# Kernel optimization log

Hardware: AMD Instinct MI355X
Metric: run time of the kernel (lower is better)

The kernel has to match this reference:

```python
import math
import jax, jax.numpy as jnp
import numpy as np

B, L, D, H = 4, 1024, 512, 8
DK = D // H

def setup_inputs() -> dict:
    key = jax.random.key(0)
    ks = jax.random.split(key, 12)
    s = 0.02
    return {
        "query": jax.random.normal(ks[0], (B, L, D), jnp.float32),
        "key": jax.random.normal(ks[1], (B, L, D), jnp.float32),
        "value": jax.random.normal(ks[2], (B, L, D), jnp.float32),
        "wq_w": jax.random.normal(ks[3], (D, D), jnp.float32) * s,
        "wq_b": jnp.zeros((D,), jnp.float32),
        "wk_w": jax.random.normal(ks[4], (D, D), jnp.float32) * s,
        "wk_b": jnp.zeros((D,), jnp.float32),
        "wv_w": jax.random.normal(ks[5], (D, D), jnp.float32) * s,
        "wv_b": jnp.zeros((D,), jnp.float32),
        "dense_w": jax.random.normal(ks[6], (D, D), jnp.float32) * s,
        "dense_b": jnp.zeros((D,), jnp.float32),
        "gate_w": jax.random.normal(ks[7], (D, 1), jnp.float32) * s,
        "gate_b": jnp.zeros((1,), jnp.float32),
        "mp_wq_w": jax.random.normal(ks[8], (D, D), jnp.float32) * s,
        "mp_wq_b": jnp.zeros((D,), jnp.float32),
        "mp_wk_w": jax.random.normal(ks[9], (D, D), jnp.float32) * s,
        "mp_wk_b": jnp.zeros((D,), jnp.float32),
    }

def reference(query, key, value, wq_w, wq_b, wk_w, wk_b, wv_w, wv_b,
              dense_w, dense_b, gate_w, gate_b,
              mp_wq_w, mp_wq_b, mp_wk_w, mp_wk_b):
    # Multi-head projections -> (B, H, L, DK)
    q = (query @ wq_w + wq_b).reshape(B, L, H, DK).transpose(0, 2, 1, 3)
    k = (key @ wk_w + wk_b).reshape(B, L, H, DK).transpose(0, 2, 1, 3)
    v = (value @ wv_w + wv_b).reshape(B, L, H, DK).transpose(0, 2, 1, 3)

    # MaskPerturbation on original (unprojected-into-heads) Q, K; scale by sqrt(d_model)
    qp = query @ mp_wq_w + mp_wq_b              # (B, L, D)
    kp = key @ mp_wk_w + mp_wk_b                # (B, L, D)
    m = jax.nn.sigmoid(jnp.einsum('bqd,bkd->bqk', qp, kp) / math.sqrt(D))  # (B, L, L)

    # Scaled dot-product attention (no mask)
    scores = jnp.einsum('bhqd,bhkd->bhqk', q, k) / math.sqrt(DK)  # (B, H, L, L)
    p_attn = jax.nn.softmax(scores, axis=-1)

    # Calibration: attn_cal = attn * exp(1 - m), combined with per-query gate, re-softmax
    attn_cal = p_attn * jnp.exp(1.0 - m[:, None])                 # (B, H, L, L)
    g = jax.nn.sigmoid(query @ gate_w + gate_b)[:, None]          # (B, 1, L, 1)
    attn_comb = g * p_attn + (1.0 - g) * attn_cal
    attn_final = jax.nn.softmax(attn_comb, axis=-1)

    out = jnp.einsum('bhqk,bhkd->bhqd', attn_final, v)            # (B, H, L, DK)
    out = out.transpose(0, 2, 1, 3).reshape(B, L, D)
    out = out @ dense_w + dense_b                                 # dropout p=0 (eval)
    return (out, m)
```

## Files before the change

### kernel.cpp

```cpp
#include <hip/hip_runtime.h>

#define B_  4
#define L_  1024
#define D_  512
#define H_  8
#define DK_ 64
#define BL_ (B_*L_)

typedef unsigned short us16;
typedef __attribute__((ext_vector_type(8))) short bf16x8;
typedef __attribute__((ext_vector_type(4))) float f32x4;

__device__ __forceinline__ float us2f(us16 u) {
  union { unsigned int i; float f; } x;
  x.i = ((unsigned int)u) << 16;
  return x.f;
}
__device__ __forceinline__ us16 f2us(float f) {
  union { float f; unsigned int i; } x;
  x.f = f;
  unsigned int r = x.i + 0x7FFFu + ((x.i >> 16) & 1u);
  return (us16)(r >> 16);
}
__device__ __forceinline__ us16 cvt_us(float f) { return f2us(f); }
__device__ __forceinline__ us16 cvt_us(us16 u) { return u; }
__device__ __forceinline__ float fexp2(float x) {
  return __builtin_amdgcn_exp2f(x);
}

#define MFMA(a, b, c) __builtin_amdgcn_mfma_f32_16x16x32_bf16(a, b, c, 0, 0, 0)

struct WT6 {
  const float* src[6];
  us16* dst[6];
};
__global__ __launch_bounds__(256) void prep(WT6 p, const float* __restrict__ query,
    const float* __restrict__ gw, const float* __restrict__ gb,
    float* __restrict__ g, us16* __restrict__ qb) {
  __shared__ us16 T[64][72];
  int id = blockIdx.x;
  const int t = threadIdx.x;
  if (id < 1024) {
    int row = id * 4 + (t >> 6);
    int lane = t & 63;
    float pz = 0.f;
    for (int d = lane; d < D_; d += 64) pz += query[(size_t)row * D_ + d] * gw[d];
#pragma unroll
    for (int off = 32; off; off >>= 1) pz += __shfl_down(pz, off);
    if (lane == 0) g[row] = 1.f / (1.f + __expf(-(pz + gb[0])));
    return;
  }
  if (id >= 1408) {
    size_t base = (size_t)(id - 1408) * 4096 + t * 16;
    const float* src = query + base;
    union { bf16x8 v; us16 u[8]; } a0, a1;
#pragma unroll
    for (int j = 0; j < 8; ++j) { a0.u[j] = f2us(src[j]); a1.u[j] = f2us(src[8 + j]); }
    *(bf16x8*)&qb[base] = a0.v;
    *(bf16x8*)&qb[base + 8] = a1.v;
    return;
  }
  id -= 1024;
  const int z = id >> 6;
  const int k0 = ((id >> 3) & 7) * 64, n0 = (id & 7) * 64;
  const float* __restrict__ W = p.src[z];
  us16* __restrict__ Wt = p.dst[z];
  {
    int r = t >> 2, c = (t & 3) * 16;
    const float* src = W + (size_t)(k0 + r) * 512 + n0 + c;
    union { bf16x8 v; us16 u[8]; } p0, p1;
#pragma unroll
    for (int j = 0; j < 8; ++j) { p0.u[j] = f2us(src[j]); p1.u[j] = f2us(src[8 + j]); }
    *(bf16x8*)&T[r][c] = p0.v;
    *(bf16x8*)&T[r][c + 8] = p1.v;
  }
  __syncthreads();
  {
    int n = t >> 2, c = (t & 3) * 16;
    union { bf16x8 v; us16 u[8]; } p0, p1;
#pragma unroll
    for (int j = 0; j < 8; ++j) { p0.u[j] = T[c + j][n]; p1.u[j] = T[c + 8 + j][n]; }
    us16* dst = Wt + (size_t)(n0 + n) * 512 + k0 + c;
    *(bf16x8*)dst = p0.v;
    *(bf16x8*)(dst + 8) = p1.v;
  }
}

__global__ __launch_bounds__(256) void gate_kernel(
    const float* __restrict__ query, const float* __restrict__ gw,
    const float* __restrict__ gb, float* __restrict__ g) {
  int row = blockIdx.x * 4 + (threadIdx.x >> 6);
  int lane = threadIdx.x & 63;
  float p = 0.f;
  for (int d = lane; d < D_; d += 64) p += query[(size_t)row * D_ + d] * gw[d];
#pragma unroll
  for (int off = 32; off; off >>= 1) p += __shfl_down(p, off);
  if (lane == 0) g[row] = 1.f / (1.f + __expf(-(p + gb[0])));
}

struct GJob {
  const float* A; const us16* Ab; const us16* Wt;
  const float* bias; us16* C; int mode; int atype;
};
struct GJobs { GJob j[3]; };

__global__ __launch_bounds__(256) void gemm3(GJobs jobs) {
  __shared__ us16 Al[64][72];
  __shared__ us16 Wl[64][72];
  int f = blockIdx.x + 8 * (blockIdx.y + 64 * blockIdx.z);
  const int cpx = 64 * (int)gridDim.z;
  f = (f & 7) * cpx + (f >> 3);
  const int bx = f & 7, by = (f >> 3) & 63, bz = f >> 9;
  const GJob J = jobs.j[bz];
  const int tid = threadIdx.x;
  const int w = tid >> 6, lane = tid & 63;
  const int quad = lane >> 4, lc = lane & 15;
  const int row0 = by * 64, col0 = bx * 64;
  const int sr = tid >> 2, sc = (tid & 3) * 16;
  f32x4 acc[4] = {};
  for (int k0 = 0; k0 < 512; k0 += 64) {
    if (J.atype) {
      const us16* as = J.Ab + (size_t)(row0 + sr) * 512 + k0 + sc;
      *(bf16x8*)&Al[sr][sc] = *(const bf16x8*)as;
      *(bf16x8*)&Al[sr][sc + 8] = *(const bf16x8*)(as + 8);
    } else {
      const float* as = J.A + (size_t)(row0 + sr) * 512 + k0 + sc;
      union { bf16x8 v; us16 u[8]; } p0, p1;
#pragma unroll
      for (int j = 0; j < 8; ++j) { p0.u[j] = f2us(as[j]); p1.u[j] = f2us(as[8 + j]); }
      *(bf16x8*)&Al[sr][sc] = p0.v;
      *(bf16x8*)&Al[sr][sc + 8] = p1.v;
    }
    {
      const us16* wsrc = J.Wt + (size_t)(col0 + sr) * 512 + k0 + sc;
      *(bf16x8*)&Wl[sr][sc] = *(const bf16x8*)wsrc;
      *(bf16x8*)&Wl[sr][sc + 8] = *(const bf16x8*)(wsrc + 8);
    }
    __syncthreads();
    bf16x8 a0 = *(const bf16x8*)&Al[w * 16 + lc][quad * 8];
    bf16x8 a1 = *(const bf16x8*)&Al[w * 16 + lc][32 + quad * 8];
#pragma unroll
    for (int ct = 0; ct < 4; ++ct) {
      bf16x8 b0 = *(const bf16x8*)&Wl[ct * 16 + lc][quad * 8];
      bf16x8 b1 = *(const bf16x8*)&Wl[ct * 16 + lc][32 + quad * 8];
      acc[ct] = MFMA(a0, b0, acc[ct]);
      acc[ct] = MFMA(a1, b1, acc[ct]);
    }
    __syncthreads();
  }
  const int orow = row0 + w * 16 + quad * 4;
#pragma unroll
  for (int ct = 0; ct < 4; ++ct) {
    const int col = col0 + ct * 16 + lc;
    const float bv = J.bias[col];
    if (J.mode == 0) {
#pragma unroll
      for (int r = 0; r < 4; ++r)
        J.C[(size_t)(orow + r) * 512 + col] = f2us(acc[ct][r] + bv);
    } else {
      const int h = col >> 6, dk = col & 63;
#pragma unroll
      for (int r = 0; r < 4; ++r) {
        const int grow = orow + r;
        const int b = grow >> 10, kv = grow & 1023;
        J.C[(((size_t)b * H_ + h) * DK_ + dk) * L_ + kv] = f2us(acc[ct][r] + bv);
      }
    }
  }
}

__global__ __launch_bounds__(256) void gemm_dense(
    const us16* __restrict__ A, const us16* __restrict__ Wt,
    const float* __restrict__ bias, float* __restrict__ C) {
  __shared__ us16 Al[64][72];
  __shared__ us16 Wl[64][72];
  int f = blockIdx.x + 8 * blockIdx.y;
  f = (f & 7) * 64 + (f >> 3);
  const int bx = f & 7, by = f >> 3;
  const int tid = threadIdx.x;
  const int w = tid >> 6, lane = tid & 63;
  const int quad = lane >> 4, lc = lane & 15;
  const int row0 = by * 64, col0 = bx * 64;
  const int sr = tid >> 2, sc = (tid & 3) * 16;
  f32x4 acc[4] = {};
  for (int k0 = 0; k0 < 512; k0 += 64) {
    const us16* as = A + (size_t)(row0 + sr) * 512 + k0 + sc;
    const us16* wsrc = Wt + (size_t)(col0 + sr) * 512 + k0 + sc;
    *(bf16x8*)&Al[sr][sc] = *(const bf16x8*)as;
    *(bf16x8*)&Al[sr][sc + 8] = *(const bf16x8*)(as + 8);
    *(bf16x8*)&Wl[sr][sc] = *(const bf16x8*)wsrc;
    *(bf16x8*)&Wl[sr][sc + 8] = *(const bf16x8*)(wsrc + 8);
    __syncthreads();
    bf16x8 a0 = *(const bf16x8*)&Al[w * 16 + lc][quad * 8];
    bf16x8 a1 = *(const bf16x8*)&Al[w * 16 + lc][32 + quad * 8];
#pragma unroll
    for (int ct = 0; ct < 4; ++ct) {
      bf16x8 b0 = *(const bf16x8*)&Wl[ct * 16 + lc][quad * 8];
      bf16x8 b1 = *(const bf16x8*)&Wl[ct * 16 + lc][32 + quad * 8];
      acc[ct] = MFMA(a0, b0, acc[ct]);
      acc[ct] = MFMA(a1, b1, acc[ct]);
    }
    __syncthreads();
  }
  const int orow = row0 + w * 16 + quad * 4;
#pragma unroll
  for (int ct = 0; ct < 4; ++ct) {
    const int col = col0 + ct * 16 + lc;
    const float bv = bias[col];
#pragma unroll
    for (int r = 0; r < 4; ++r)
      C[(size_t)(orow + r) * 512 + col] = acc[ct][r] + bv;
  }
}

template <bool WK>
__global__ __launch_bounds__(256) void mask16(
    const us16* __restrict__ QP, const us16* __restrict__ KP,
    float* __restrict__ Mout, const float* __restrict__ gbuf,
    us16* __restrict__ Wk) {
  __shared__ us16 Al[64][72];
  __shared__ us16 Bl[64][72];
  int f = blockIdx.x + 16 * (blockIdx.y + 16 * blockIdx.z);
  f = (f & 7) * 128 + (f >> 3);
  const int bx = f & 15, by = (f >> 4) & 15, b = f >> 8;
  const int tid = threadIdx.x;
  const int w = tid >> 6, lane = tid & 63;
  const int quad = lane >> 4, lc = lane & 15;
  const int row0 = by * 64, col0 = bx * 64;
  const us16* Ab = QP + (size_t)b * L_ * D_;
  const us16* Bb = KP + (size_t)b * L_ * D_;
  const int sr = tid >> 2, sc = (tid & 3) * 16;
  f32x4 acc[4] = {};
  for (int k0 = 0; k0 < 512; k0 += 64) {
    {
      const us16* as = Ab + (size_t)(row0 + sr) * 512 + k0 + sc;
      *(bf16x8*)&Al[sr][sc] = *(const bf16x8*)as;
      *(bf16x8*)&Al[sr][sc + 8] = *(const bf16x8*)(as + 8);
    }
    {
      const us16* bs = Bb + (size_t)(col0 + sr) * 512 + k0 + sc;
      *(bf16x8*)&Bl[sr][sc] = *(const bf16x8*)bs;
      *(bf16x8*)&Bl[sr][sc + 8] = *(const bf16x8*)(bs + 8);
    }
    __syncthreads();
    bf16x8 a0 = *(const bf16x8*)&Al[w * 16 + lc][quad * 8];
    bf16x8 a1 = *(const bf16x8*)&Al[w * 16 + lc][32 + quad * 8];
#pragma unroll
    for (int ct = 0; ct < 4; ++ct) {
      bf16x8 b0 = *(const bf16x8*)&Bl[ct * 16 + lc][quad * 8];
      bf16x8 b1 = *(const bf16x8*)&Bl[ct * 16 + lc][32 + quad * 8];
      acc[ct] = MFMA(a0, b0, acc[ct]);
      acc[ct] = MFMA(a1, b1, acc[ct]);
    }
    __syncthreads();
  }
  const float sc2 = 0.04419417382415922f;
  const int orow = row0 + w * 16 + quad * 4;
  float gq[4];
  if (WK) {
#pragma unroll
    for (int r = 0; r < 4; ++r) gq[r] = gbuf[b * L_ + orow + r];
  }
#pragma unroll
  for (int ct = 0; ct < 4; ++ct) {
    const int col = col0 + ct * 16 + lc;
#pragma unroll
    for (int r = 0; r < 4; ++r) {
      float x = acc[ct][r] * sc2;
      float v = 1.f / (1.f + __expf(-x));
      size_t idx = ((size_t)b * L_ + orow + r) * L_ + col;
      Mout[idx] = v;
      if (WK) Wk[idx] = f2us(gq[r] + (1.f - gq[r]) * __expf(1.f - v));
    }
  }
}

typedef const __attribute__((address_space(1))) unsigned int* gas_u32;
typedef __attribute__((address_space(3))) unsigned int* las_u32;

__global__ __launch_bounds__(256, 4) void attn8(
    const us16* Qp, const us16* __restrict__ Kp,
    const us16* __restrict__ Vt, const us16* __restrict__ Wk, us16* O) {
  __shared__ us16 P[16 * 1032];
  __shared__ float red[2][4][16];
  const int tid = threadIdx.x;
  const int w = tid >> 6, lane = tid & 63;
  const int quad = lane >> 4, lc = lane & 15;
  int raw = blockIdx.x + 64 * (blockIdx.y + 8 * blockIdx.z);
  const int c = raw & 7;
  const int rest = raw >> 3;
  const int gg = c * 4 + (rest & 3);
  const int q0 = (rest >> 2) * 16;
  const int h = gg & 7, b = gg >> 3;

  const us16* qptr = Qp + (size_t)(b * L_ + q0 + lc) * D_ + h * DK_;
  bf16x8 qa0 = *(const bf16x8*)(qptr + quad * 8);
  bf16x8 qa1 = *(const bf16x8*)(qptr + 32 + quad * 8);

  const us16* Kbase = Kp + (size_t)b * L_ * D_ + h * DK_;
  const int srow = lane >> 3;
  const int sblk = ((lane & 7) ^ srow) * 8;
  us16* kst = &P[w * 4096];

  auto stage = [&](int kt, int d) {
#pragma unroll
    for (int i = 0; i < 2; ++i) {
      const us16* src =
          Kbase + (size_t)(kt * 64 + w * 16 + i * 8 + srow) * D_ + sblk;
      __builtin_amdgcn_global_load_lds(
          (gas_u32)src, (las_u32)(kst + d * 1024 + i * 512), 16, 0, 0);
    }
  };

  const float c1 = 0.18033688011112042f;

  stage(0, 0); stage(1, 1); stage(2, 2); stage(3, 3);

  float s[16][4];
  float sm[4] = {0.f, 0.f, 0.f, 0.f};
#pragma unroll
  for (int kt = 0; kt < 16; ++kt) {
    const int d = kt & 3;
    if (kt <= 12)      asm volatile("s_waitcnt vmcnt(6)" ::: "memory");
    else if (kt == 13) asm volatile("s_waitcnt vmcnt(4)" ::: "memory");
    else if (kt == 14) asm volatile("s_waitcnt vmcnt(2)" ::: "memory");
    else               asm volatile("s_waitcnt vmcnt(0)" ::: "memory");
    __builtin_amdgcn_sched_barrier(0);
    bf16x8 b0 = *(const bf16x8*)&kst[d * 1024 + lc * 64 + ((quad ^ (lc & 7)) * 8)];
    bf16x8 b1 = *(const bf16x8*)&kst[d * 1024 + lc * 64 + (((4 + quad) ^ (lc & 7)) * 8)];
    if (kt + 4 < 16) stage(kt + 4, d);
    f32x4 a = {};
    __builtin_amdgcn_s_setprio(1);
    a = MFMA(qa0, b0, a);
    a = MFMA(qa1, b1, a);
    __builtin_amdgcn_s_setprio(0);
#pragma unroll
    for (int r = 0; r < 4; ++r) {
      float e = fexp2(a[r] * c1);
      s[kt][r] = e;
      sm[r] += e;
    }
    __builtin_amdgcn_sched_barrier(0);
  }
#pragma unroll
  for (int r = 0; r < 4; ++r)
#pragma unroll
    for (int off = 1; off < 16; off <<= 1) sm[r] += __shfl_xor(sm[r], off);
  if (lc == 0)
#pragma unroll
    for (int r = 0; r < 4; ++r) red[0][w][quad * 4 + r] = sm[r];
  __syncthreads();
  float invr[4];
#pragma unroll
  for (int r = 0; r < 4; ++r) {
    const int row = quad * 4 + r;
    invr[r] = 1.44269504088896341f /
              (red[0][0][row] + red[0][1][row] + red[0][2][row] + red[0][3][row]);
  }

  const us16* wkb = Wk + (size_t)(b * L_ + q0 + quad * 4) * L_ + w * 16 + lc;
  float ts[4] = {0.f, 0.f, 0.f, 0.f};
#pragma unroll
  for (int kt = 0; kt < 16; ++kt) {
#pragma unroll
    for (int r = 0; r < 4; ++r) {
      float cv = s[kt][r] * invr[r] * us2f(wkb[(size_t)r * L_ + kt * 64]);
      float e2 = fexp2(cv);
      ts[r] += e2;
      P[(quad * 4 + r) * 1032 + kt * 64 + w * 16 + lc] = f2us(e2);
    }
  }
#pragma unroll
  for (int r = 0; r < 4; ++r)
#pragma unroll
    for (int off = 1; off < 16; off <<= 1) ts[r] += __shfl_xor(ts[r], off);
  if (lc == 0)
#pragma unroll
    for (int r = 0; r < 4; ++r) red[1][w][quad * 4 + r] = ts[r];
  __syncthreads();

  const us16* Vb = Vt + ((size_t)(b * H_ + h) * DK_ + w * 16 + lc) * L_;
  f32x4 oacc = {};
  for (int kv = 0; kv < L_; kv += 32) {
    bf16x8 pa = *(const bf16x8*)&P[lc * 1032 + kv + quad * 8];
    bf16x8 vb = *(const bf16x8*)(Vb + kv + quad * 8);
    __builtin_amdgcn_s_setprio(1);
    oacc = MFMA(pa, vb, oacc);
    __builtin_amdgcn_s_setprio(0);
  }
#pragma unroll
  for (int r = 0; r < 4; ++r) {
    const int row = quad * 4 + r;
    float inv2 = 1.f /
        (red[1][0][row] + red[1][1][row] + red[1][2][row] + red[1][3][row]);
    O[(size_t)(b * L_ + q0 + row) * D_ + h * DK_ + w * 16 + lc] =
        f2us(oacc[r] * inv2);
  }
}

template <int MODE, typename TA>
__global__ __launch_bounds__(256) void gemm16(
    const TA* __restrict__ A, const float* __restrict__ W,
    const float* __restrict__ bias, void* __restrict__ Cout) {
  __shared__ us16 Al[64][56];
  __shared__ us16 Wl[64][56];
  const int tid = threadIdx.x;
  const int w = tid >> 6, lane = tid & 63;
  const int quad = lane >> 4, lc = lane & 15;
  const int row0 = blockIdx.y * 64, col0 = blockIdx.x * 64;
  f32x4 acc[4] = {};
  const int arow = tid >> 2, aks = (tid & 3) * 8;
  const int wk = tid & 31, wns = (tid >> 5) * 8;
  for (int k0 = 0; k0 < 512; k0 += 32) {
    {
      union { bf16x8 v; us16 u[8]; } pk;
      const TA* src = A + (size_t)(row0 + arow) * 512 + k0 + aks;
#pragma unroll
      for (int j = 0; j < 8; ++j) pk.u[j] = cvt_us(src[j]);
      *(bf16x8*)&Al[arow][aks] = pk.v;
    }
    {
      const float* src = W + (size_t)(k0 + wk) * 512 + col0 + wns;
#pragma unroll
      for (int j = 0; j < 8; ++j) Wl[wns + j][wk] = f2us(src[j]);
    }
    __syncthreads();
    bf16x8 af = *(const bf16x8*)&Al[w * 16 + lc][quad * 8];
#pragma unroll
    for (int ct = 0; ct < 4; ++ct) {
      bf16x8 bf = *(const bf16x8*)&Wl[ct * 16 + lc][quad * 8];
      acc[ct] = MFMA(af, bf, acc[ct]);
    }
    __syncthreads();
  }
  const int orow = row0 + w * 16 + quad * 4;
#pragma unroll
  for (int ct = 0; ct < 4; ++ct) {
    const int col = col0 + ct * 16 + lc;
    const float bv = bias[col];
    if (MODE == 0) {
      us16* C = (us16*)Cout;
#pragma unroll
      for (int r = 0; r < 4; ++r)
        C[(size_t)(orow + r) * 512 + col] = f2us(acc[ct][r] + bv);
    } else if (MODE == 1) {
      us16* C = (us16*)Cout;
      const int h = col >> 6, dk = col & 63;
#pragma unroll
      for (int r = 0; r < 4; ++r) {
        const int grow = orow + r;
        const int b = grow >> 10, kv = grow & 1023;
        C[(((size_t)b * H_ + h) * DK_ + dk) * L_ + kv] = f2us(acc[ct][r] + bv);
      }
    } else {
      float* C = (float*)Cout;
#pragma unroll
      for (int r = 0; r < 4; ++r)
        C[(size_t)(orow + r) * 512 + col] = acc[ct][r] + bv;
    }
  }
}

__global__ __launch_bounds__(256, 3) void attn2_fb(
    const us16* Qp, const us16* __restrict__ Kp,
    const us16* __restrict__ Vt, const float* __restrict__ Mm,
    const float* __restrict__ gbuf, us16* O) {
  __shared__ us16 Ql[16][72];
  __shared__ us16 P[16 * 1032];
  __shared__ float red[2][4][16];
  const int tid = threadIdx.x;
  const int w = tid >> 6, lane = tid & 63;
  const int quad = lane >> 4, lc = lane & 15;
  const int b = blockIdx.z, h = blockIdx.y, q0 = blockIdx.x * 16;
  if (tid < 128) {
    int r = tid >> 3, ks = (tid & 7) * 8;
    *(bf16x8*)&Ql[r][ks] =
        *(const bf16x8*)(Qp + (size_t)(b * L_ + q0 + r) * D_ + h * DK_ + ks);
  }
  __syncthreads();
  bf16x8 qa0 = *(const bf16x8*)&Ql[lc][quad * 8];
  bf16x8 qa1 = *(const bf16x8*)&Ql[lc][32 + quad * 8];
  const us16* Kbase = Kp + (size_t)b * L_ * D_ + h * DK_;
  float s[16][4];
#pragma unroll
  for (int kt = 0; kt < 16; ++kt) {
    const us16* kr = Kbase + (size_t)(kt * 64 + w * 16 + lc) * D_;
    bf16x8 b0 = *(const bf16x8*)(kr + quad * 8);
    bf16x8 b1 = *(const bf16x8*)(kr + 32 + quad * 8);
    f32x4 a = {};
    a = MFMA(qa0, b0, a);
    a = MFMA(qa1, b1, a);
#pragma unroll
    for (int r = 0; r < 4; ++r) s[kt][r] = a[r] * 0.125f;
  }
  float sm[4];
#pragma unroll
  for (int r = 0; r < 4; ++r) {
    float t = 0.f;
#pragma unroll
    for (int kt = 0; kt < 16; ++kt) { s[kt][r] = __expf(s[kt][r]); t += s[kt][r]; }
#pragma unroll
    for (int off = 1; off < 16; off <<= 1) t += __shfl_xor(t, off);
    sm[r] = t;
  }
  if (lc == 0)
#pragma unroll
    for (int r = 0; r < 4; ++r) red[0][w][quad * 4 + r] = sm[r];
  __syncthreads();
  float inv[4];
#pragma unroll
  for (int r = 0; r < 4; ++r) {
    const int row = quad * 4 + r;
    inv[r] = 1.f / (red[0][0][row] + red[0][1][row] + red[0][2][row] + red[0][3][row]);
  }
  float gq[4];
#pragma unroll
  for (int r = 0; r < 4; ++r) gq[r] = gbuf[b * L_ + q0 + quad * 4 + r];
#pragma unroll
  for (int r = 0; r < 4; ++r) {
    const float* mrow = Mm + (size_t)(b * L_ + q0 + quad * 4 + r) * L_;
    float t = 0.f;
#pragma unroll
    for (int kt = 0; kt < 16; ++kt) {
      float mval = mrow[kt * 64 + w * 16 + lc];
      float c = s[kt][r] * inv[r] * (gq[r] + (1.f - gq[r]) * __expf(1.f - mval));
      float e = __expf(c);
      s[kt][r] = e;
      t += e;
    }
#pragma unroll
    for (int off = 1; off < 16; off <<= 1) t += __shfl_xor(t, off);
    sm[r] = t;
  }
  if (lc == 0)
#pragma unroll
    for (int r = 0; r < 4; ++r) red[1][w][quad * 4 + r] = sm[r];
  __syncthreads();
#pragma unroll
  for (int r = 0; r < 4; ++r) {
    const int row = quad * 4 + r;
    inv[r] = 1.f / (red[1][0][row] + red[1][1][row] + red[1][2][row] + red[1][3][row]);
  }
#pragma unroll
  for (int kt = 0; kt < 16; ++kt)
#pragma unroll
    for (int r = 0; r < 4; ++r)
      P[(quad * 4 + r) * 1032 + kt * 64 + w * 16 + lc] = f2us(s[kt][r] * inv[r]);
  __syncthreads();
  const us16* Vb = Vt + (size_t)(b * H_ + h) * DK_ * L_;
  f32x4 oacc = {};
  for (int kv = 0; kv < L_; kv += 32) {
    bf16x8 pa = *(const bf16x8*)&P[lc * 1032 + kv + quad * 8];
    bf16x8 vb = *(const bf16x8*)(Vb + (size_t)(w * 16 + lc) * L_ + kv + quad * 8);
    oacc = MFMA(pa, vb, oacc);
  }
#pragma unroll
  for (int r = 0; r < 4; ++r)
    O[(size_t)(b * L_ + q0 + quad * 4 + r) * D_ + h * DK_ + w * 16 + lc] =
        f2us(oacc[r]);
}

extern "C" void kernel_launch(void* const* d_in, const int* in_sizes, int n_in,
                              void* d_out, int out_size, void* d_ws, size_t ws_size,
                              hipStream_t stream) {
  const float* query   = (const float*)d_in[0];
  const float* key     = (const float*)d_in[1];
  const float* value   = (const float*)d_in[2];
  const float* wq_w    = (const float*)d_in[3];
  const float* wq_b    = (const float*)d_in[4];
  const float* wk_w    = (const float*)d_in[5];
  const float* wk_b    = (const float*)d_in[6];
  const float* wv_w    = (const float*)d_in[7];
  const float* wv_b    = (const float*)d_in[8];
  const float* dense_w = (const float*)d_in[9];
  const float* dense_b = (const float*)d_in[10];
  const float* gate_w  = (const float*)d_in[11];
  const float* gate_b  = (const float*)d_in[12];
  const float* mp_wq_w = (const float*)d_in[13];
  const float* mp_wq_b = (const float*)d_in[14];
  const float* mp_wk_w = (const float*)d_in[15];
  const float* mp_wk_b = (const float*)d_in[16];

  const size_t RSZ = (size_t)BL_ * D_;
  const size_t WSZ = (size_t)D_ * D_;
  us16* R0 = (us16*)d_ws;
  us16* R1 = R0 + RSZ;

  float* out0 = (float*)d_out;
  float* outm = out0 + (size_t)B_ * L_ * D_;
  us16*  Vt   = (us16*)d_out;

  dim3 blk(256);

  if (ws_size >= ((size_t)20 << 20)) {
    us16* Wt0 = R1 + RSZ;
    us16* mpq_t = Wt0;
    us16* mpk_t = Wt0 + WSZ;
    us16* wq_t  = Wt0 + 2 * WSZ;
    us16* wk_t  = Wt0 + 3 * WSZ;
    us16* wv_t  = Wt0 + 4 * WSZ;
    us16* dw_t  = Wt0 + 5 * WSZ;
    us16* Wk    = Wt0 + 6 * WSZ;
    float* gbuf = (float*)(Wk + (size_t)B_ * L_ * L_);
    us16* qb = (us16*)((char*)d_out + (4u << 20));

    WT6 wt;
    wt.src[0] = mp_wq_w; wt.dst[0] = mpq_t;
    wt.src[1] = mp_wk_w; wt.dst[1] = mpk_t;
    wt.src[2] = wq_w;    wt.dst[2] = wq_t;
    wt.src[3] = wk_w;    wt.dst[3] = wk_t;
    wt.src[4] = wv_w;    wt.dst[4] = wv_t;
    wt.src[5] = dense_w; wt.dst[5] = dw_t;
    hipLaunchKernelGGL(prep, dim3(1920), blk, 0, stream, wt, query, gate_w, gate_b, gbuf, qb);

    GJobs mp;
    mp.j[0] = { nullptr, qb, mpq_t, mp_wq_b, R0, 0, 1 };
    mp.j[1] = { key, nullptr, mpk_t, mp_wk_b, R1, 0, 0 };
    mp.j[2] = mp.j[1];
    hipLaunchKernelGGL(gemm3, dim3(8, 64, 2), blk, 0, stream, mp);
    hipLaunchKernelGGL(mask16<true>, dim3(16, 16, B_), blk, 0, stream,
                       R0, R1, outm, gbuf, Wk);

    GJobs qkv;
    qkv.j[0] = { nullptr, qb, wq_t, wq_b, R0, 0, 1 };
    qkv.j[1] = { key, nullptr, wk_t, wk_b, R1, 0, 0 };
    qkv.j[2] = { value, nullptr, wv_t, wv_b, Vt, 1, 0 };
    hipLaunchKernelGGL(gemm3, dim3(8, 64, 3), blk, 0, stream, qkv);

    hipLaunchKernelGGL(attn8, dim3(L_ / 16, H_, B_), blk, 0, stream, R0, R1, Vt, Wk, R0);
    hipLaunchKernelGGL(gemm_dense, dim3(8, 64), blk, 0, stream, R0, dw_t, dense_b, out0);
  } else {
    float* gbuf = (float*)((char*)d_out + (4u << 20));
    dim3 gproj(8, 64);
    hipLaunchKernelGGL((gemm16<0, float>), gproj, blk, 0, stream, query, mp_wq_w, mp_wq_b, (void*)R0);
    hipLaunchKernelGGL((gemm16<0, float>), gproj, blk, 0, stream, key,   mp_wk_w, mp_wk_b, (void*)R1);
    hipLaunchKernelGGL(mask16<false>, dim3(16, 16, B_), blk, 0, stream,
                       R0, R1, outm, (const float*)nullptr, (us16*)nullptr);
    hipLaunchKernelGGL((gemm16<0, float>), gproj, blk, 0, stream, query, wq_w, wq_b, (void*)R0);
    hipLaunchKernelGGL((gemm16<0, float>), gproj, blk, 0, stream, key,   wk_w, wk_b, (void*)R1);
    hipLaunchKernelGGL((gemm16<1, float>), gproj, blk, 0, stream, value, wv_w, wv_b, (void*)Vt);
    hipLaunchKernelGGL(gate_kernel, dim3(BL_ / 4), blk, 0, stream, query, gate_w, gate_b, gbuf);
    hipLaunchKernelGGL(attn2_fb, dim3(L_ / 16, H_, B_), blk, 0, stream, R0, R1, Vt, outm, gbuf, R0);
    hipLaunchKernelGGL((gemm16<2, us16>), gproj, blk, 0, stream, R0, dense_w, dense_b, (void*)out0);
  }
}
```

Baseline: 222.1 us.

## Double-buffer GEMM tiles with async global-to-LDS loads and XOR swizzle

```diff
diff --git a/kernel.cpp b/kernel.cpp
--- a/kernel.cpp
+++ b/kernel.cpp
@@ -29,6 +29,18 @@
 }
 
 #define MFMA(a, b, c) __builtin_amdgcn_mfma_f32_16x16x32_bf16(a, b, c, 0, 0, 0)
+
+typedef const __attribute__((address_space(1))) unsigned int* gas_u32;
+typedef __attribute__((address_space(3))) unsigned int* las_u32;
+
+__device__ __forceinline__ void stg8(const us16* rowbase, us16* dst, int lane) {
+  const us16* src = rowbase + (size_t)(lane >> 3) * 512 +
+                    (((lane & 7) ^ (lane >> 3)) * 8);
+  __builtin_amdgcn_global_load_lds((gas_u32)src, (las_u32)dst, 16, 0, 0);
+}
+__device__ __forceinline__ bf16x8 rdz(const us16* buf, int row, int blk) {
+  return *(const bf16x8*)&buf[row * 64 + ((blk ^ (row & 7)) * 8)];
+}
 
 struct WT6 {
   const float* src[6];
@@ -105,8 +117,8 @@
 struct GJobs { GJob j[3]; };
 
 __global__ __launch_bounds__(256) void gemm3(GJobs jobs) {
-  __shared__ us16 Al[64][72];
-  __shared__ us16 Wl[64][72];
+  __shared__ us16 Abuf[2][64 * 64];
+  __shared__ us16 Bbuf[2][64 * 64];
   int f = blockIdx.x + 8 * (blockIdx.y + 64 * blockIdx.z);
   const int cpx = 64 * (int)gridDim.z;
   f = (f & 7) * cpx + (f >> 3);
@@ -116,37 +128,93 @@
   const int w = tid >> 6, lane = tid & 63;
   const int quad = lane >> 4, lc = lane & 15;
   const int row0 = by * 64, col0 = bx * 64;
-  const int sr = tid >> 2, sc = (tid & 3) * 16;
   f32x4 acc[4] = {};
-  for (int k0 = 0; k0 < 512; k0 += 64) {
-    if (J.atype) {
-      const us16* as = J.Ab + (size_t)(row0 + sr) * 512 + k0 + sc;
-      *(bf16x8*)&Al[sr][sc] = *(const bf16x8*)as;
-      *(bf16x8*)&Al[sr][sc + 8] = *(const bf16x8*)(as + 8);
-    } else {
-      const float* as = J.A + (size_t)(row0 + sr) * 512 + k0 + sc;
-      union { bf16x8 v; us16 u[8]; } p0, p1;
-#pragma unroll
-      for (int j = 0; j < 8; ++j) { p0.u[j] = f2us(as[j]); p1.u[j] = f2us(as[8 + j]); }
-      *(bf16x8*)&Al[sr][sc] = p0.v;
-      *(bf16x8*)&Al[sr][sc + 8] = p1.v;
-    }
-    {
-      const us16* wsrc = J.Wt + (size_t)(col0 + sr) * 512 + k0 + sc;
-      *(bf16x8*)&Wl[sr][sc] = *(const bf16x8*)wsrc;
-      *(bf16x8*)&Wl[sr][sc + 8] = *(const bf16x8*)(wsrc + 8);
-    }
-    __syncthreads();
-    bf16x8 a0 = *(const bf16x8*)&Al[w * 16 + lc][quad * 8];
-    bf16x8 a1 = *(const bf16x8*)&Al[w * 16 + lc][32 + quad * 8];
-#pragma unroll
-    for (int ct = 0; ct < 4; ++ct) {
-      bf16x8 b0 = *(const bf16x8*)&Wl[ct * 16 + lc][quad * 8];
-      bf16x8 b1 = *(const bf16x8*)&Wl[ct * 16 + lc][32 + quad * 8];
-      acc[ct] = MFMA(a0, b0, acc[ct]);
-      acc[ct] = MFMA(a1, b1, acc[ct]);
-    }
-    __syncthreads();
+
+  const us16* Bg = J.Wt + (size_t)(col0 + w * 16) * 512;
+  auto stgB = [&](int k, int cur) {
+    stg8(Bg + k * 64, &Bbuf[cur][(w * 16) * 64], lane);
+    stg8(Bg + 8 * 512 + k * 64, &Bbuf[cur][(w * 16 + 8) * 64], lane);
+  };
+
+  if (J.atype) {
+    const us16* Ag = J.Ab + (size_t)(row0 + w * 16) * 512;
+    auto stgA = [&](int k, int cur) {
+      stg8(Ag + k * 64, &Abuf[cur][(w * 16) * 64], lane);
+      stg8(Ag + 8 * 512 + k * 64, &Abuf[cur][(w * 16 + 8) * 64], lane);
+    };
+    stgA(0, 0); stgB(0, 0);
+    stgA(1, 1); stgB(1, 1);
+#pragma unroll
+    for (int k = 0; k < 8; ++k) {
+      const int cur = k & 1;
+      if (k < 7) asm volatile("s_waitcnt vmcnt(4)" ::: "memory");
+      else       asm volatile("s_waitcnt vmcnt(0)" ::: "memory");
+      __builtin_amdgcn_sched_barrier(0);
+      __builtin_amdgcn_s_barrier();
+      __builtin_amdgcn_sched_barrier(0);
+      bf16x8 a0 = rdz(Abuf[cur], w * 16 + lc, quad);
+      bf16x8 a1 = rdz(Abuf[cur], w * 16 + lc, 4 + quad);
+#pragma unroll
+      for (int ct = 0; ct < 4; ++ct) {
+        bf16x8 b0 = rdz(Bbuf[cur], ct * 16 + lc, quad);
+        bf16x8 b1 = rdz(Bbuf[cur], ct * 16 + lc, 4 + quad);
+        acc[ct] = MFMA(a0, b0, acc[ct]);
+        acc[ct] = MFMA(a1, b1, acc[ct]);
+      }
+      __builtin_amdgcn_sched_barrier(0);
+      __builtin_amdgcn_s_barrier();
+      __builtin_amdgcn_sched_barrier(0);
+      if (k + 2 < 8) { stgA(k + 2, cur); stgB(k + 2, cur); }
+    }
+  } else {
+    const int fr = tid >> 2, j0 = (tid & 3) * 2;
+    const float* arow = J.A + (size_t)(row0 + fr) * 512 + j0 * 8;
+    f32x4 vA[4], vB[4];
+    auto ldA = [&](int k, f32x4* v) {
+      const float* p = arow + k * 64;
+      v[0] = *(const f32x4*)(p);
+      v[1] = *(const f32x4*)(p + 4);
+      v[2] = *(const f32x4*)(p + 8);
+      v[3] = *(const f32x4*)(p + 12);
+    };
+    auto wrA = [&](us16* abuf, const f32x4* v) {
+      union { bf16x8 x; us16 u[8]; } p0, p1;
+#pragma unroll
+      for (int j = 0; j < 4; ++j) {
+        p0.u[j] = f2us(v[0][j]); p0.u[4 + j] = f2us(v[1][j]);
+        p1.u[j] = f2us(v[2][j]); p1.u[4 + j] = f2us(v[3][j]);
+      }
+      us16* wp = abuf + fr * 64;
+      *(bf16x8*)&wp[(j0 ^ (fr & 7)) * 8] = p0.x;
+      *(bf16x8*)&wp[((j0 + 1) ^ (fr & 7)) * 8] = p1.x;
+    };
+    ldA(0, vA); stgB(0, 0);
+    ldA(1, vB); stgB(1, 1);
+#pragma unroll
+    for (int k = 0; k < 8; ++k) {
+      const int cur = k & 1;
+      if (k < 7) asm volatile("s_waitcnt vmcnt(6)" ::: "memory");
+      else       asm volatile("s_waitcnt vmcnt(0)" ::: "memory");
+      __builtin_amdgcn_sched_barrier(0);
+      wrA(&Abuf[cur][0], cur ? vB : vA);
+      asm volatile("s_waitcnt lgkmcnt(0)" ::: "memory");
+      __builtin_amdgcn_sched_barrier(0);
+      __builtin_amdgcn_s_barrier();
+      __builtin_amdgcn_sched_barrier(0);
+      bf16x8 a0 = rdz(Abuf[cur], w * 16 + lc, quad);
+      bf16x8 a1 = rdz(Abuf[cur], w * 16 + lc, 4 + quad);
+#pragma unroll
+      for (int ct = 0; ct < 4; ++ct) {
+        bf16x8 b0 = rdz(Bbuf[cur], ct * 16 + lc, quad);
+        bf16x8 b1 = rdz(Bbuf[cur], ct * 16 + lc, 4 + quad);
+        acc[ct] = MFMA(a0, b0, acc[ct]);
+        acc[ct] = MFMA(a1, b1, acc[ct]);
+      }
+      __builtin_amdgcn_sched_barrier(0);
+      __builtin_amdgcn_s_barrier();
+      __builtin_amdgcn_sched_barrier(0);
+      if (k + 2 < 8) { ldA(k + 2, cur ? vB : vA); stgB(k + 2, cur); }
+    }
   }
   const int orow = row0 + w * 16 + quad * 4;
 #pragma unroll
@@ -172,8 +240,8 @@
 __global__ __launch_bounds__(256) void gemm_dense(
     const us16* __restrict__ A, const us16* __restrict__ Wt,
     const float* __restrict__ bias, float* __restrict__ C) {
-  __shared__ us16 Al[64][72];
-  __shared__ us16 Wl[64][72];
+  __shared__ us16 Abuf[2][64 * 64];
+  __shared__ us16 Bbuf[2][64 * 64];
   int f = blockIdx.x + 8 * blockIdx.y;
   f = (f & 7) * 64 + (f >> 3);
   const int bx = f & 7, by = f >> 3;
@@ -181,26 +249,37 @@
   const int w = tid >> 6, lane = tid & 63;
   const int quad = lane >> 4, lc = lane & 15;
   const int row0 = by * 64, col0 = bx * 64;
-  const int sr = tid >> 2, sc = (tid & 3) * 16;
   f32x4 acc[4] = {};
-  for (int k0 = 0; k0 < 512; k0 += 64) {
-    const us16* as = A + (size_t)(row0 + sr) * 512 + k0 + sc;
-    const us16* wsrc = Wt + (size_t)(col0 + sr) * 512 + k0 + sc;
-    *(bf16x8*)&Al[sr][sc] = *(const bf16x8*)as;
-    *(bf16x8*)&Al[sr][sc + 8] = *(const bf16x8*)(as + 8);
-    *(bf16x8*)&Wl[sr][sc] = *(const bf16x8*)wsrc;
-    *(bf16x8*)&Wl[sr][sc + 8] = *(const bf16x8*)(wsrc + 8);
-    __syncthreads();
-    bf16x8 a0 = *(const bf16x8*)&Al[w * 16 + lc][quad * 8];
-    bf16x8 a1 = *(const bf16x8*)&Al[w * 16 + lc][32 + quad * 8];
+  const us16* Ag = A + (size_t)(row0 + w * 16) * 512;
+  const us16* Bg = Wt + (size_t)(col0 + w * 16) * 512;
+  auto stg = [&](int k, int cur) {
+    stg8(Ag + k * 64, &Abuf[cur][(w * 16) * 64], lane);
+    stg8(Ag + 8 * 512 + k * 64, &Abuf[cur][(w * 16 + 8) * 64], lane);
+    stg8(Bg + k * 64, &Bbuf[cur][(w * 16) * 64], lane);
+    stg8(Bg + 8 * 512 + k * 64, &Bbuf[cur][(w * 16 + 8) * 64], lane);
+  };
+  stg(0, 0); stg(1, 1);
+#pragma unroll
+  for (int k = 0; k < 8; ++k) {
+    const int cur = k & 1;
+    if (k < 7) asm volatile("s_waitcnt vmcnt(4)" ::: "memory");
+    else       asm volatile("s_waitcnt vmcnt(0)" ::: "memory");
+    __builtin_amdgcn_sched_barrier(0);
+    __builtin_amdgcn_s_barrier();
+    __builtin_amdgcn_sched_barrier(0);
+    bf16x8 a0 = rdz(Abuf[cur], w * 16 + lc, quad);
+    bf16x8 a1 = rdz(Abuf[cur], w * 16 + lc, 4 + quad);
 #pragma unroll
     for (int ct = 0; ct < 4; ++ct) {
-      bf16x8 b0 = *(const bf16x8*)&Wl[ct * 16 + lc][quad * 8];
-      bf16x8 b1 = *(const bf16x8*)&Wl[ct * 16 + lc][32 + quad * 8];
+      bf16x8 b0 = rdz(Bbuf[cur], ct * 16 + lc, quad);
+      bf16x8 b1 = rdz(Bbuf[cur], ct * 16 + lc, 4 + quad);
       acc[ct] = MFMA(a0, b0, acc[ct]);
       acc[ct] = MFMA(a1, b1, acc[ct]);
     }
-    __syncthreads();
+    __builtin_amdgcn_sched_barrier(0);
+    __builtin_amdgcn_s_barrier();
+    __builtin_amdgcn_sched_barrier(0);
+    if (k + 2 < 8) stg(k + 2, cur);
   }
   const int orow = row0 + w * 16 + quad * 4;
 #pragma unroll
@@ -218,8 +297,8 @@
     const us16* __restrict__ QP, const us16* __restrict__ KP,
     float* __restrict__ Mout, const float* __restrict__ gbuf,
     us16* __restrict__ Wk) {
-  __shared__ us16 Al[64][72];
-  __shared__ us16 Bl[64][72];
+  __shared__ us16 Abuf[2][64 * 64];
+  __shared__ us16 Bbuf[2][64 * 64];
   int f = blockIdx.x + 16 * (blockIdx.y + 16 * blockIdx.z);
   f = (f & 7) * 128 + (f >> 3);
   const int bx = f & 15, by = (f >> 4) & 15, b = f >> 8;
@@ -227,32 +306,37 @@
   const int w = tid >> 6, lane = tid & 63;
   const int quad = lane >> 4, lc = lane & 15;
   const int row0 = by * 64, col0 = bx * 64;
-  const us16* Ab = QP + (size_t)b * L_ * D_;
-  const us16* Bb = KP + (size_t)b * L_ * D_;
-  const int sr = tid >> 2, sc = (tid & 3) * 16;
   f32x4 acc[4] = {};
-  for (int k0 = 0; k0 < 512; k0 += 64) {
-    {
-      const us16* as = Ab + (size_t)(row0 + sr) * 512 + k0 + sc;
-      *(bf16x8*)&Al[sr][sc] = *(const bf16x8*)as;
-      *(bf16x8*)&Al[sr][sc + 8] = *(const bf16x8*)(as + 8);
-    }
-    {
-      const us16* bs = Bb + (size_t)(col0 + sr) * 512 + k0 + sc;
-      *(bf16x8*)&Bl[sr][sc] = *(const bf16x8*)bs;
-      *(bf16x8*)&Bl[sr][sc + 8] = *(const bf16x8*)(bs + 8);
-    }
-    __syncthreads();
-    bf16x8 a0 = *(const bf16x8*)&Al[w * 16 + lc][quad * 8];
-    bf16x8 a1 = *(const bf16x8*)&Al[w * 16 + lc][32 + quad * 8];
+  const us16* Ag = QP + (size_t)b * L_ * D_ + (size_t)(row0 + w * 16) * 512;
+  const us16* Bg = KP + (size_t)b * L_ * D_ + (size_t)(col0 + w * 16) * 512;
+  auto stg = [&](int k, int cur) {
+    stg8(Ag + k * 64, &Abuf[cur][(w * 16) * 64], lane);
+    stg8(Ag + 8 * 512 + k * 64, &Abuf[cur][(w * 16 + 8) * 64], lane);
+    stg8(Bg + k * 64, &Bbuf[cur][(w * 16) * 64], lane);
+    stg8(Bg + 8 * 512 + k * 64, &Bbuf[cur][(w * 16 + 8) * 64], lane);
+  };
+  stg(0, 0); stg(1, 1);
+#pragma unroll
+  for (int k = 0; k < 8; ++k) {
+    const int cur = k & 1;
+    if (k < 7) asm volatile("s_waitcnt vmcnt(4)" ::: "memory");
+    else       asm volatile("s_waitcnt vmcnt(0)" ::: "memory");
+    __builtin_amdgcn_sched_barrier(0);
+    __builtin_amdgcn_s_barrier();
+    __builtin_amdgcn_sched_barrier(0);
+    bf16x8 a0 = rdz(Abuf[cur], w * 16 + lc, quad);
+    bf16x8 a1 = rdz(Abuf[cur], w * 16 + lc, 4 + quad);
 #pragma unroll
     for (int ct = 0; ct < 4; ++ct) {
-      bf16x8 b0 = *(const bf16x8*)&Bl[ct * 16 + lc][quad * 8];
-      bf16x8 b1 = *(const bf16x8*)&Bl[ct * 16 + lc][32 + quad * 8];
+      bf16x8 b0 = rdz(Bbuf[cur], ct * 16 + lc, quad);
+      bf16x8 b1 = rdz(Bbuf[cur], ct * 16 + lc, 4 + quad);
       acc[ct] = MFMA(a0, b0, acc[ct]);
       acc[ct] = MFMA(a1, b1, acc[ct]);
     }
-    __syncthreads();
+    __builtin_amdgcn_sched_barrier(0);
+    __builtin_amdgcn_s_barrier();
+    __builtin_amdgcn_sched_barrier(0);
+    if (k + 2 < 8) stg(k + 2, cur);
   }
   const float sc2 = 0.04419417382415922f;
   const int orow = row0 + w * 16 + quad * 4;
@@ -274,9 +358,6 @@
     }
   }
 }
-
-typedef const __attribute__((address_space(1))) unsigned int* gas_u32;
-typedef __attribute__((address_space(3))) unsigned int* las_u32;
 
 __global__ __launch_bounds__(256, 4) void attn8(
     const us16* Qp, const us16* __restrict__ Kp,
```

Result: faster. 208.0 us (-6.4%).
